# Performance work log

Measured on AMD Instinct MI355X. Metric: run time of the kernel, lower is better.

## Reference

```python
import jax, jax.numpy as jnp
import numpy as np

B, S, H, D, P = 16, 512, 12, 768, 256
TOP_RATE = 0.1
K = int(round(TOP_RATE * S))  # 51, matches round(self.top_rate * hidden_state.size(1))
LN_EPS = 1e-5


def setup_inputs() -> dict:
    key = jax.random.key(0)
    ks = jax.random.split(key, 6)
    return {
        "hidden_state": jax.random.normal(ks[0], (B, S, D), dtype=jnp.float32),
        "attention": jax.random.normal(ks[1], (B, H, S, S), dtype=jnp.float32),
        "length": S,  # uniform valid length (scalar int)
        # node_trans: Linear(D, P)
        "W_node": jax.random.normal(ks[2], (D, P), dtype=jnp.float32) * 0.02,
        "b_node": jnp.zeros((P,), dtype=jnp.float32),
        # node_eta parameter, initialized to 0 (self.node_eta.data.fill_(0))
        "node_eta": jnp.zeros((1,), dtype=jnp.float32),
        # fc: Linear(P, P)
        "W_fc": jax.random.normal(ks[3], (P, P), dtype=jnp.float32) * 0.02,
        "b_fc": jnp.zeros((P,), dtype=jnp.float32),
        # LayerNorm(P)
        "ln_gamma": jnp.ones((P,), dtype=jnp.float32),
        "ln_beta": jnp.zeros((P,), dtype=jnp.float32),
    }


def reference(hidden_state, attention, W_node, b_node, node_eta, W_fc, b_fc,
              ln_gamma, ln_beta, length):
    # average attention over heads: [B, S, S]
    avg_atten = attention.mean(axis=1)
    # per-target-node top-k neighbors
    vals, idx = jax.lax.top_k(avg_atten, K)  # [B, S, K]
    # edge mask replicating softmax(where(v>0, v, -1e9)) followed by nonzero():
    # entries at -1e9 underflow to exactly 0 in fp32 softmax iff the row has a
    # positive value; otherwise the softmax is uniform and all edges survive.
    keep = vals > 0.0
    row_has_pos = keep.any(axis=-1, keepdims=True)
    keep = jnp.where(row_has_pos, keep, True)            # [B, S, K] (>=1 True per row)
    keepf = keep.astype(hidden_state.dtype)[..., None]   # [B, S, K, 1]

    # node_trans on all nodes: [B, S, P]
    h = hidden_state @ W_node + b_node

    # gather source-node features h[b, idx[b, t, j], :] -> [B, S, K, P]
    gathered = jax.vmap(lambda hb, ib: hb[ib])(h, idx)

    # reduce='mean': edge weight w=1, mailbox mean over kept incoming edges
    h_agg = (gathered * keepf).sum(axis=2) / keepf.sum(axis=2)

    eta = node_eta[0]
    new_h = eta * h + (1.0 - eta) * h_agg                # [B, S, P]

    # dgl.mean_nodes: mean over the `length` nodes of each sub-graph (=S here)
    out = new_h.mean(axis=1)                             # [B, P]

    # fc(dropout(tanh(out))) with dropout in eval mode (identity)
    out = jnp.tanh(out) @ W_fc + b_fc

    # LayerNorm
    mu = out.mean(axis=-1, keepdims=True)
    var = ((out - mu) ** 2).mean(axis=-1, keepdims=True)
    out = (out - mu) / jnp.sqrt(var + LN_EPS) * ln_gamma + ln_beta
    return out
```

## Files before the change

### kernel.cpp

```cpp
#include <hip/hip_runtime.h>
#include <math.h>

#define B_ 16
#define S_ 512
#define H_ 12
#define D_ 768
#define P_ 256
#define K_ 51
#define CH_ 16
#define NCHUNK_ (S_/CH_)

__device__ __forceinline__ unsigned okey(float f) {
  unsigned u = __float_as_uint(f);
  return (u & 0x80000000u) ? ~u : (u | 0x80000000u);
}

__global__ __launch_bounds__(256) void k1_topk_weights(
    const float* __restrict__ attn, float* __restrict__ w) {
  const int bt = blockIdx.x;
  const int b = bt >> 9;
  const int t = bt & (S_ - 1);
  const int tid = threadIdx.x;
  const int wave = tid >> 6;

  __shared__ unsigned keys[S_];
  __shared__ __align__(16) unsigned hist[2][4][256];
  __shared__ int ipar[4];

  ((uint4*)&hist[0][0][0])[tid] = uint4{0u, 0u, 0u, 0u};
  if (tid == 0) ipar[0] = 0;

  const float* base = attn + (((size_t)b * H_) * S_ + t) * S_;
  float2 acc = make_float2(0.f, 0.f);
  #pragma unroll
  for (int h = 0; h < H_; ++h) {
    const float2 v = *(const float2*)(base + (size_t)h * S_ * S_ + 2 * tid);
    acc.x += v.x; acc.y += v.y;
  }
  const float a0 = acc.x * (1.0f / (float)H_);
  const float a1 = acc.y * (1.0f / (float)H_);
  const unsigned k0 = okey(a0);
  const unsigned k1v = okey(a1);
  keys[2 * tid] = k0;
  keys[2 * tid + 1] = k1v;

  {
    const unsigned long long m0 = __ballot(a0 > 0.f);
    const unsigned long long m1 = __ballot(a1 > 0.f);
    if ((tid & 63) == 0) atomicAdd(&ipar[0], __popcll(m0) + __popcll(m1));
  }
  __syncthreads();
  const int p = ipar[0];

  bool sel0, sel1;
  float invcnt;
  if (p >= 1 && p < K_) {
    sel0 = (a0 > 0.f);
    sel1 = (a1 > 0.f);
    invcnt = 1.0f / (float)p;
  } else {
    unsigned prefix = 0;
    int remaining = K_;
    int tieCnt = 0;
    int exited = 0;
    unsigned exitm = 0;
    for (int pass = 0; pass < 4; ++pass) {
      const int shift = 24 - 8 * pass;
      const unsigned pm = (pass == 0) ? 0u : (0xFFFFFFFFu << (shift + 8));
      const int cur = pass & 1, nxt = cur ^ 1;
      if ((k0 & pm) == prefix) atomicAdd(&hist[cur][wave][(k0 >> shift) & 255u], 1u);
      if ((k1v & pm) == prefix) atomicAdd(&hist[cur][wave][(k1v >> shift) & 255u], 1u);
      ((uint4*)&hist[nxt][0][0])[tid] = uint4{0u, 0u, 0u, 0u};
      __syncthreads();
      if (wave == 0) {
        const int lane = tid;
        unsigned c0 = 0, c1 = 0, c2 = 0, c3 = 0;
        #pragma unroll
        for (int wv = 0; wv < 4; ++wv) {
          const uint4 v = ((const uint4*)&hist[cur][wv][0])[lane];
          c0 += v.x; c1 += v.y; c2 += v.z; c3 += v.w;
        }
        const unsigned loc = c0 + c1 + c2 + c3;
        unsigned suf = loc;
        #pragma unroll
        for (int off = 1; off < 64; off <<= 1) {
          const unsigned v = __shfl_down(suf, off, 64);
          if (lane + off < 64) suf += v;
        }
        const unsigned after = suf - loc;
        const unsigned s3 = after + c3;
        const unsigned s2 = s3 + c2;
        const unsigned s1 = s2 + c1;
        const unsigned s0 = s1 + c0;
        const unsigned rem = (unsigned)remaining;
        if (s0 >= rem && s1 < rem)    { ipar[1] = 4*lane+0; ipar[2] = (int)s1;    ipar[3] = (int)(s0 - s1); }
        if (s1 >= rem && s2 < rem)    { ipar[1] = 4*lane+1; ipar[2] = (int)s2;    ipar[3] = (int)(s1 - s2); }
        if (s2 >= rem && s3 < rem)    { ipar[1] = 4*lane+2; ipar[2] = (int)s3;    ipar[3] = (int)(s2 - s3); }
        if (s3 >= rem && after < rem) { ipar[1] = 4*lane+3; ipar[2] = (int)after; ipar[3] = (int)(s3 - after); }
      }
      __syncthreads();
      const int dc = ipar[1];
      prefix |= ((unsigned)dc) << shift;
      remaining -= ipar[2];
      tieCnt = ipar[3];
      if (tieCnt == remaining) {
        exited = 1;
        exitm = 0xFFFFFFFFu << shift;
        break;
      }
    }
    if (exited) {
      sel0 = (k0 & exitm) >= prefix;
      sel1 = (k1v & exitm) >= prefix;
    } else {
      const unsigned T = prefix;
      sel0 = (k0 > T);
      sel1 = (k1v > T);
      if (k0 == T) {
        int r = 0;
        for (int s2i = 0; s2i < 2 * tid; ++s2i) r += (keys[s2i] == T);
        if (r < remaining) sel0 = true;
      }
      if (k1v == T) {
        int r = 0;
        for (int s2i = 0; s2i < 2 * tid + 1; ++s2i) r += (keys[s2i] == T);
        if (r < remaining) sel1 = true;
      }
    }
    invcnt = 1.0f / (float)K_;
  }

  float* wrow = w + b * S_;
  if (sel0) atomicAdd(&wrow[2 * tid], invcnt);
  if (sel1) atomicAdd(&wrow[2 * tid + 1], invcnt);
}

__global__ __launch_bounds__(192) void k2_weighted_sum(
    const float* __restrict__ hidden, const float* __restrict__ w,
    const float* __restrict__ node_eta, float* __restrict__ x) {
  const int chunk = blockIdx.x;
  const int b = blockIdx.y;
  const int tid = threadIdx.x;
  __shared__ float coef[CH_];
  if (tid < CH_) {
    const float eta = node_eta[0];
    const float wv = w[b * S_ + chunk * CH_ + tid];
    coef[tid] = (eta + (1.0f - eta) * wv) * (1.0f / (float)S_);
  }
  __syncthreads();
  const float* hb = hidden + ((size_t)b * S_ + (size_t)chunk * CH_) * D_ + 4 * tid;
  float4 acc = make_float4(0.f, 0.f, 0.f, 0.f);
  #pragma unroll
  for (int s = 0; s < CH_; ++s) {
    const float4 v = *(const float4*)(hb + (size_t)s * D_);
    const float c = coef[s];
    acc.x += c * v.x; acc.y += c * v.y; acc.z += c * v.z; acc.w += c * v.w;
  }
  float* xp = x + b * D_ + 4 * tid;
  atomicAdd(xp + 0, acc.x);
  atomicAdd(xp + 1, acc.y);
  atomicAdd(xp + 2, acc.z);
  atomicAdd(xp + 3, acc.w);
}

__global__ __launch_bounds__(256) void k3_final(
    const float* __restrict__ x, const float* __restrict__ W_node,
    const float* __restrict__ b_node, const float* __restrict__ W_fc,
    const float* __restrict__ b_fc, const float* __restrict__ gamma,
    const float* __restrict__ beta, float* __restrict__ out) {
  const int b = blockIdx.x;
  const int tid = threadIdx.x;
  __shared__ float xs[D_];
  __shared__ float ts[P_];
  __shared__ float red[4];

  for (int d = tid; d < D_; d += 256) xs[d] = x[b * D_ + d];
  __syncthreads();

  float v = b_node[tid];
  #pragma unroll 8
  for (int d = 0; d < D_; ++d) v += xs[d] * W_node[d * P_ + tid];
  ts[tid] = tanhf(v);
  __syncthreads();

  float o = b_fc[tid];
  #pragma unroll 8
  for (int q = 0; q < P_; ++q) o += ts[q] * W_fc[q * P_ + tid];

  float s = o;
  #pragma unroll
  for (int off = 32; off > 0; off >>= 1) s += __shfl_down(s, off, 64);
  const int wave = tid >> 6, lane = tid & 63;
  if (lane == 0) red[wave] = s;
  __syncthreads();
  const float mu = (red[0] + red[1] + red[2] + red[3]) * (1.0f / (float)P_);
  __syncthreads();
  const float dv = o - mu;
  float s2 = dv * dv;
  #pragma unroll
  for (int off = 32; off > 0; off >>= 1) s2 += __shfl_down(s2, off, 64);
  if (lane == 0) red[wave] = s2;
  __syncthreads();
  const float var = (red[0] + red[1] + red[2] + red[3]) * (1.0f / (float)P_);
  const float inv = 1.0f / sqrtf(var + 1e-5f);
  out[b * P_ + tid] = dv * inv * gamma[tid] + beta[tid];
}

extern "C" void kernel_launch(void* const* d_in, const int* in_sizes, int n_in,
                              void* d_out, int out_size, void* d_ws, size_t ws_size,
                              hipStream_t stream) {
  (void)in_sizes; (void)n_in; (void)out_size; (void)ws_size;
  const float* hidden   = (const float*)d_in[0];
  const float* attn     = (const float*)d_in[1];
  const float* W_node   = (const float*)d_in[3];
  const float* b_node   = (const float*)d_in[4];
  const float* node_eta = (const float*)d_in[5];
  const float* W_fc     = (const float*)d_in[6];
  const float* b_fc     = (const float*)d_in[7];
  const float* gamma    = (const float*)d_in[8];
  const float* beta     = (const float*)d_in[9];
  float* out = (float*)d_out;

  float* w = (float*)d_ws;
  float* x = w + B_ * S_;
  hipMemsetAsync(d_ws, 0, (size_t)(B_ * S_ + B_ * D_) * sizeof(float), stream);

  k1_topk_weights<<<B_ * S_, 256, 0, stream>>>(attn, w);
  k2_weighted_sum<<<dim3(NCHUNK_, B_), 192, 0, stream>>>(hidden, w, node_eta, x);
  k3_final<<<B_, 256, 0, stream>>>(x, W_node, b_node, W_fc, b_fc, gamma, beta, out);
}
```

Measured before the change: 381.4 us.

## Use one wave per top-k row and split final matvecs across blocks

The top-k kernel now gives each row to one 64-lane wave instead of a 256-thread block. It uses per-wave histograms, wave ballots and shuffles in place of block barriers and shared-memory broadcast, and replaces the serial tie-rank scan with ballot popcounts. The single-block-per-batch final kernel is split into three launches: a matvec with tanh spread over 8 column blocks, an fc matvec over 4 blocks, and a LayerNorm kernel. This raises parallelism in the tail. The price is two extra launches, and the wave-level code depends on lgkmcnt waits for LDS ordering.

New measurement: 340.7 us. 1.12x faster.

```diff
diff --git a/kernel.cpp b/kernel.cpp
--- a/kernel.cpp
+++ b/kernel.cpp
@@ -10,6 +10,8 @@
 #define CH_ 16
 #define NCHUNK_ (S_/CH_)
 
+#define WAVE_SYNC() asm volatile("s_waitcnt lgkmcnt(0)" ::: "memory")
+
 __device__ __forceinline__ unsigned okey(float f) {
   unsigned u = __float_as_uint(f);
   return (u & 0x80000000u) ? ~u : (u | 0x80000000u);
@@ -17,122 +19,134 @@
 
 __global__ __launch_bounds__(256) void k1_topk_weights(
     const float* __restrict__ attn, float* __restrict__ w) {
-  const int bt = blockIdx.x;
+  const int tid = threadIdx.x;
+  const int wv = tid >> 6;
+  const int lane = tid & 63;
+  const int bt = blockIdx.x * 4 + wv;
   const int b = bt >> 9;
   const int t = bt & (S_ - 1);
-  const int tid = threadIdx.x;
-  const int wave = tid >> 6;
-
-  __shared__ unsigned keys[S_];
-  __shared__ __align__(16) unsigned hist[2][4][256];
-  __shared__ int ipar[4];
-
-  ((uint4*)&hist[0][0][0])[tid] = uint4{0u, 0u, 0u, 0u};
-  if (tid == 0) ipar[0] = 0;
+
+  __shared__ __align__(16) unsigned hist[4][256];
+
+  *(uint4*)&hist[wv][4 * lane] = uint4{0u, 0u, 0u, 0u};
 
   const float* base = attn + (((size_t)b * H_) * S_ + t) * S_;
-  float2 acc = make_float2(0.f, 0.f);
+  float a[8] = {0.f, 0.f, 0.f, 0.f, 0.f, 0.f, 0.f, 0.f};
   #pragma unroll
   for (int h = 0; h < H_; ++h) {
-    const float2 v = *(const float2*)(base + (size_t)h * S_ * S_ + 2 * tid);
-    acc.x += v.x; acc.y += v.y;
-  }
-  const float a0 = acc.x * (1.0f / (float)H_);
-  const float a1 = acc.y * (1.0f / (float)H_);
-  const unsigned k0 = okey(a0);
-  const unsigned k1v = okey(a1);
-  keys[2 * tid] = k0;
-  keys[2 * tid + 1] = k1v;
-
-  {
-    const unsigned long long m0 = __ballot(a0 > 0.f);
-    const unsigned long long m1 = __ballot(a1 > 0.f);
-    if ((tid & 63) == 0) atomicAdd(&ipar[0], __popcll(m0) + __popcll(m1));
-  }
-  __syncthreads();
-  const int p = ipar[0];
-
-  bool sel0, sel1;
+    const float* r = base + (size_t)h * (S_ * S_);
+    const float4 u = *(const float4*)(r + 4 * lane);
+    const float4 v = *(const float4*)(r + 256 + 4 * lane);
+    a[0] += u.x; a[1] += u.y; a[2] += u.z; a[3] += u.w;
+    a[4] += v.x; a[5] += v.y; a[6] += v.z; a[7] += v.w;
+  }
+  unsigned k[8];
+  #pragma unroll
+  for (int i = 0; i < 8; ++i) {
+    a[i] *= (1.0f / (float)H_);
+    k[i] = okey(a[i]);
+  }
+
+  int p = 0;
+  #pragma unroll
+  for (int i = 0; i < 8; ++i) p += __popcll(__ballot(a[i] > 0.f));
+
+  bool sel[8];
   float invcnt;
   if (p >= 1 && p < K_) {
-    sel0 = (a0 > 0.f);
-    sel1 = (a1 > 0.f);
+    #pragma unroll
+    for (int i = 0; i < 8; ++i) sel[i] = (a[i] > 0.f);
     invcnt = 1.0f / (float)p;
   } else {
     unsigned prefix = 0;
     int remaining = K_;
     int tieCnt = 0;
-    int exited = 0;
+    bool exited = false;
     unsigned exitm = 0;
     for (int pass = 0; pass < 4; ++pass) {
       const int shift = 24 - 8 * pass;
       const unsigned pm = (pass == 0) ? 0u : (0xFFFFFFFFu << (shift + 8));
-      const int cur = pass & 1, nxt = cur ^ 1;
-      if ((k0 & pm) == prefix) atomicAdd(&hist[cur][wave][(k0 >> shift) & 255u], 1u);
-      if ((k1v & pm) == prefix) atomicAdd(&hist[cur][wave][(k1v >> shift) & 255u], 1u);
-      ((uint4*)&hist[nxt][0][0])[tid] = uint4{0u, 0u, 0u, 0u};
-      __syncthreads();
-      if (wave == 0) {
-        const int lane = tid;
-        unsigned c0 = 0, c1 = 0, c2 = 0, c3 = 0;
-        #pragma unroll
-        for (int wv = 0; wv < 4; ++wv) {
-          const uint4 v = ((const uint4*)&hist[cur][wv][0])[lane];
-          c0 += v.x; c1 += v.y; c2 += v.z; c3 += v.w;
-        }
-        const unsigned loc = c0 + c1 + c2 + c3;
-        unsigned suf = loc;
-        #pragma unroll
-        for (int off = 1; off < 64; off <<= 1) {
-          const unsigned v = __shfl_down(suf, off, 64);
-          if (lane + off < 64) suf += v;
-        }
-        const unsigned after = suf - loc;
-        const unsigned s3 = after + c3;
-        const unsigned s2 = s3 + c2;
-        const unsigned s1 = s2 + c1;
-        const unsigned s0 = s1 + c0;
-        const unsigned rem = (unsigned)remaining;
-        if (s0 >= rem && s1 < rem)    { ipar[1] = 4*lane+0; ipar[2] = (int)s1;    ipar[3] = (int)(s0 - s1); }
-        if (s1 >= rem && s2 < rem)    { ipar[1] = 4*lane+1; ipar[2] = (int)s2;    ipar[3] = (int)(s1 - s2); }
-        if (s2 >= rem && s3 < rem)    { ipar[1] = 4*lane+2; ipar[2] = (int)s3;    ipar[3] = (int)(s2 - s3); }
-        if (s3 >= rem && after < rem) { ipar[1] = 4*lane+3; ipar[2] = (int)after; ipar[3] = (int)(s3 - after); }
+      WAVE_SYNC();
+      #pragma unroll
+      for (int i = 0; i < 8; ++i)
+        if ((k[i] & pm) == prefix)
+          atomicAdd(&hist[wv][(k[i] >> shift) & 255u], 1u);
+      WAVE_SYNC();
+      const uint4 c4 = *(uint4*)&hist[wv][4 * lane];
+      *(uint4*)&hist[wv][4 * lane] = uint4{0u, 0u, 0u, 0u};
+      const unsigned loc = c4.x + c4.y + c4.z + c4.w;
+      unsigned suf = loc;
+      #pragma unroll
+      for (int off = 1; off < 64; off <<= 1) {
+        const unsigned vv = __shfl_down(suf, off, 64);
+        if (lane + off < 64) suf += vv;
       }
-      __syncthreads();
-      const int dc = ipar[1];
-      prefix |= ((unsigned)dc) << shift;
-      remaining -= ipar[2];
-      tieCnt = ipar[3];
+      const unsigned after = suf - loc;
+      const unsigned s3 = after + c4.w;
+      const unsigned s2 = s3 + c4.z;
+      const unsigned s1 = s2 + c4.y;
+      const unsigned s0 = s1 + c4.x;
+      const unsigned rem = (unsigned)remaining;
+      int dig = 0, abv = 0, tie = 0;
+      bool found = false;
+      if (s0 >= rem && s1 < rem)         { dig = 4*lane+0; abv = (int)s1;    tie = (int)(s0 - s1);    found = true; }
+      else if (s1 >= rem && s2 < rem)    { dig = 4*lane+1; abv = (int)s2;    tie = (int)(s1 - s2);    found = true; }
+      else if (s2 >= rem && s3 < rem)    { dig = 4*lane+2; abv = (int)s3;    tie = (int)(s2 - s3);    found = true; }
+      else if (s3 >= rem && after < rem) { dig = 4*lane+3; abv = (int)after; tie = (int)(s3 - after); found = true; }
+      const unsigned long long fm = __ballot(found);
+      const int src = __ffsll((unsigned long long)fm) - 1;
+      dig = __shfl(dig, src, 64);
+      abv = __shfl(abv, src, 64);
+      tie = __shfl(tie, src, 64);
+      prefix |= ((unsigned)dig) << shift;
+      remaining -= abv;
+      tieCnt = tie;
       if (tieCnt == remaining) {
-        exited = 1;
-        exitm = 0xFFFFFFFFu << shift;
+        exited = true;
+        exitm = (shift == 0) ? 0xFFFFFFFFu : (0xFFFFFFFFu << shift);
         break;
       }
     }
     if (exited) {
-      sel0 = (k0 & exitm) >= prefix;
-      sel1 = (k1v & exitm) >= prefix;
+      #pragma unroll
+      for (int i = 0; i < 8; ++i) sel[i] = (k[i] & exitm) >= prefix;
     } else {
       const unsigned T = prefix;
-      sel0 = (k0 > T);
-      sel1 = (k1v > T);
-      if (k0 == T) {
-        int r = 0;
-        for (int s2i = 0; s2i < 2 * tid; ++s2i) r += (keys[s2i] == T);
-        if (r < remaining) sel0 = true;
-      }
-      if (k1v == T) {
-        int r = 0;
-        for (int s2i = 0; s2i < 2 * tid + 1; ++s2i) r += (keys[s2i] == T);
-        if (r < remaining) sel1 = true;
+      unsigned long long m[8];
+      #pragma unroll
+      for (int i = 0; i < 8; ++i) m[i] = __ballot(k[i] == T);
+      const unsigned long long lt = ((unsigned long long)1 << lane) - 1ull;
+      int fh = 0;
+      #pragma unroll
+      for (int i = 0; i < 4; ++i) fh += __popcll(m[i]);
+      #pragma unroll
+      for (int i = 0; i < 8; ++i) {
+        sel[i] = (k[i] > T);
+        if (k[i] == T) {
+          int r = 0;
+          if (i < 4) {
+            #pragma unroll
+            for (int i2 = 0; i2 < 4; ++i2) r += __popcll(m[i2] & lt);
+            for (int i2 = 0; i2 < i; ++i2) r += (int)((m[i2] >> lane) & 1ull);
+          } else {
+            r = fh;
+            #pragma unroll
+            for (int i2 = 4; i2 < 8; ++i2) r += __popcll(m[i2] & lt);
+            for (int i2 = 4; i2 < i; ++i2) r += (int)((m[i2] >> lane) & 1ull);
+          }
+          if (r < remaining) sel[i] = true;
+        }
       }
     }
     invcnt = 1.0f / (float)K_;
   }
 
   float* wrow = w + b * S_;
-  if (sel0) atomicAdd(&wrow[2 * tid], invcnt);
-  if (sel1) atomicAdd(&wrow[2 * tid + 1], invcnt);
+  #pragma unroll
+  for (int i = 0; i < 8; ++i) {
+    const int col = (i < 4) ? (4 * lane + i) : (256 + 4 * lane + (i - 4));
+    if (sel[i]) atomicAdd(&wrow[col], invcnt);
+  }
 }
 
 __global__ __launch_bounds__(192) void k2_weighted_sum(
@@ -163,30 +177,79 @@
   atomicAdd(xp + 3, acc.w);
 }
 
-__global__ __launch_bounds__(256) void k3_final(
+__global__ __launch_bounds__(256) void k3a_tanh_matvec(
     const float* __restrict__ x, const float* __restrict__ W_node,
-    const float* __restrict__ b_node, const float* __restrict__ W_fc,
-    const float* __restrict__ b_fc, const float* __restrict__ gamma,
+    const float* __restrict__ b_node, float* __restrict__ tbuf) {
+  const int j = blockIdx.x;
+  const int b = blockIdx.y;
+  const int tid = threadIdx.x;
+  const int pp = tid & 15;
+  const int g = tid >> 4;
+  __shared__ float xs[D_];
+  __shared__ float part[16][32];
+  for (int d = tid; d < D_; d += 256) xs[d] = x[b * D_ + d];
+  __syncthreads();
+  const float* Wp = W_node + 32 * j + 2 * pp;
+  float2 acc = make_float2(0.f, 0.f);
+  const int d0 = 48 * g;
+  #pragma unroll 8
+  for (int dd = 0; dd < 48; ++dd) {
+    const int d = d0 + dd;
+    const float2 wv = *(const float2*)(Wp + (size_t)d * P_);
+    const float xv = xs[d];
+    acc.x += xv * wv.x; acc.y += xv * wv.y;
+  }
+  *(float2*)&part[g][2 * pp] = acc;
+  __syncthreads();
+  if (tid < 32) {
+    float s = 0.f;
+    #pragma unroll
+    for (int gg = 0; gg < 16; ++gg) s += part[gg][tid];
+    const int pcol = 32 * j + tid;
+    tbuf[b * P_ + pcol] = tanhf(s + b_node[pcol]);
+  }
+}
+
+__global__ __launch_bounds__(256) void k3b_fc(
+    const float* __restrict__ tbuf, const float* __restrict__ W_fc,
+    const float* __restrict__ b_fc, float* __restrict__ obuf) {
+  const int j = blockIdx.x;
+  const int b = blockIdx.y;
+  const int tid = threadIdx.x;
+  const int pp = tid & 31;
+  const int g = tid >> 5;
+  __shared__ float ts[P_];
+  __shared__ float part[8][64];
+  ts[tid] = tbuf[b * P_ + tid];
+  __syncthreads();
+  const float* Wp = W_fc + 64 * j + 2 * pp;
+  float2 acc = make_float2(0.f, 0.f);
+  const int q0 = 32 * g;
+  #pragma unroll 8
+  for (int qq = 0; qq < 32; ++qq) {
+    const int q = q0 + qq;
+    const float2 wv = *(const float2*)(Wp + (size_t)q * P_);
+    const float tv = ts[q];
+    acc.x += tv * wv.x; acc.y += tv * wv.y;
+  }
+  *(float2*)&part[g][2 * pp] = acc;
+  __syncthreads();
+  if (tid < 64) {
+    float s = 0.f;
+    #pragma unroll
+    for (int gg = 0; gg < 8; ++gg) s += part[gg][tid];
+    const int pcol = 64 * j + tid;
+    obuf[b * P_ + pcol] = s + b_fc[pcol];
+  }
+}
+
+__global__ __launch_bounds__(256) void k3c_layernorm(
+    const float* __restrict__ obuf, const float* __restrict__ gamma,
     const float* __restrict__ beta, float* __restrict__ out) {
   const int b = blockIdx.x;
   const int tid = threadIdx.x;
-  __shared__ float xs[D_];
-  __shared__ float ts[P_];
   __shared__ float red[4];
-
-  for (int d = tid; d < D_; d += 256) xs[d] = x[b * D_ + d];
-  __syncthreads();
-
-  float v = b_node[tid];
-  #pragma unroll 8
-  for (int d = 0; d < D_; ++d) v += xs[d] * W_node[d * P_ + tid];
-  ts[tid] = tanhf(v);
-  __syncthreads();
-
-  float o = b_fc[tid];
-  #pragma unroll 8
-  for (int q = 0; q < P_; ++q) o += ts[q] * W_fc[q * P_ + tid];
-
+  const float o = obuf[b * P_ + tid];
   float s = o;
   #pragma unroll
   for (int off = 32; off > 0; off >>= 1) s += __shfl_down(s, off, 64);
@@ -221,11 +284,15 @@
   const float* beta     = (const float*)d_in[9];
   float* out = (float*)d_out;
 
-  float* w = (float*)d_ws;
-  float* x = w + B_ * S_;
+  float* w    = (float*)d_ws;
+  float* x    = w + B_ * S_;
+  float* tbuf = x + B_ * D_;
+  float* obuf = tbuf + B_ * P_;
   hipMemsetAsync(d_ws, 0, (size_t)(B_ * S_ + B_ * D_) * sizeof(float), stream);
 
-  k1_topk_weights<<<B_ * S_, 256, 0, stream>>>(attn, w);
+  k1_topk_weights<<<(B_ * S_) / 4, 256, 0, stream>>>(attn, w);
   k2_weighted_sum<<<dim3(NCHUNK_, B_), 192, 0, stream>>>(hidden, w, node_eta, x);
-  k3_final<<<B_, 256, 0, stream>>>(x, W_node, b_node, W_fc, b_fc, gamma, beta, out);
-}
+  k3a_tanh_matvec<<<dim3(8, B_), 256, 0, stream>>>(x, W_node, b_node, tbuf);
+  k3b_fc<<<dim3(4, B_), 256, 0, stream>>>(tbuf, W_fc, b_fc, obuf);
+  k3c_layernorm<<<B_, 256, 0, stream>>>(obuf, gamma, beta, out);
+}
```
